# Optimization experiments

Hardware: AMD Instinct MI355X
Metric: run time of the kernel (lower is better)

The kernel has to match this reference:

```python
import jax, jax.numpy as jnp
import numpy as np

DEPTH = 2
TWO_PI = 6.283185307179586


def _apply_ry(state, theta, axis):
    """Apply RY(theta) on qubit at `axis` of state [N,2,2,2,2]. theta: [N] or scalar."""
    half = theta * 0.5
    a0 = jnp.take(state, 0, axis=axis)  # [N,2,2,2]
    a1 = jnp.take(state, 1, axis=axis)
    c = jnp.reshape(jnp.cos(half), (-1,) + (1,) * (a0.ndim - 1))
    s = jnp.reshape(jnp.sin(half), (-1,) + (1,) * (a0.ndim - 1))
    return jnp.stack([c * a0 - s * a1, s * a0 + c * a1], axis=axis)


def _apply_cnot(state, c_axis, t_axis):
    a0 = jnp.take(state, 0, axis=c_axis)  # control=0: unchanged
    a1 = jnp.take(state, 1, axis=c_axis)  # control=1: flip target
    t_ax = t_axis - (1 if t_axis > c_axis else 0)
    a1 = jnp.flip(a1, axis=t_ax)
    return jnp.stack([a0, a1], axis=c_axis)


def _simulate(patches, weights):
    """patches: [N,4] angles. Returns <Z_i> for i=0..3, shape [N,4]. All gates real."""
    N = patches.shape[0]
    state = jnp.zeros((N, 2, 2, 2, 2), dtype=patches.dtype)
    state = state.at[:, 0, 0, 0, 0].set(1.0)
    for w in range(4):  # data encoding
        state = _apply_ry(state, patches[:, w], axis=w + 1)
    for d in range(DEPTH):  # variational layers
        for w in range(4):
            state = _apply_ry(state, weights[d, w], axis=w + 1)
        for c, t in ((0, 1), (1, 2), (2, 3)):
            state = _apply_cnot(state, c + 1, t + 1)
    probs = state * state
    zs = []
    for w in range(4):
        p0 = jnp.take(probs, 0, axis=w + 1).sum(axis=(1, 2, 3))
        p1 = jnp.take(probs, 1, axis=w + 1).sum(axis=(1, 2, 3))
        zs.append(p0 - p1)
    return jnp.stack(zs, axis=-1)  # [N,4]


def setup_inputs() -> dict:
    key = jax.random.key(0)
    k1, k2, k3, k4 = jax.random.split(key, 4)
    B = 8192
    x = jax.random.uniform(k1, (B, 1, 28, 28), dtype=jnp.float32)
    weights = jax.random.uniform(k2, (DEPTH, 4), dtype=jnp.float32) * TWO_PI
    W = jax.random.normal(k3, (10, 4 * 14 * 14), dtype=jnp.float32) * 0.02
    b = jax.random.normal(k4, (10,), dtype=jnp.float32) * 0.02
    return {"x": x, "weights": weights, "W": W, "b": b}


def reference(x, weights, W, b):
    B = x.shape[0]
    # Extract non-overlapping 2x2 patches in row-major (i,j) order;
    # within a patch, order is [(i,j),(i,j+1),(i+1,j),(i+1,j+1)] matching x[:,:,i:i+2,j:j+2].view(B,4)
    p = x.reshape(B, 14, 2, 14, 2).transpose(0, 1, 3, 2, 4).reshape(B, 196, 4)
    feats = _simulate(p.reshape(B * 196, 4), weights).reshape(B, 196 * 4)
    logits = feats @ W.T + b
    return jax.nn.log_softmax(logits, axis=-1)
```

## Files before the change

### kernel.cpp

```cpp
#include <hip/hip_runtime.h>
#include <math.h>

#define INV2PI 0.15915494309189535f

__device__ __forceinline__ float rfl(float v) {
    return __int_as_float(__builtin_amdgcn_readfirstlane(__float_as_int(v)));
}

__global__ __launch_bounds__(256) void quanv_wave_kernel(
    const float* __restrict__ x,
    const float* __restrict__ wts,
    const float* __restrict__ W,
    const float* __restrict__ bias,
    float* __restrict__ out,
    int B)
{
    const int lane = threadIdx.x & 63;
    const int img  = blockIdx.x * 4 + (threadIdx.x >> 6);
    if (img >= B) return;

    float w0r[4], cw1[4], sw1[4];
#pragma unroll
    for (int q = 0; q < 4; ++q) {
        w0r[q] = rfl(wts[q] * INV2PI);
        float r = wts[4 + q] * INV2PI;
        r -= floorf(r);
        cw1[q] = __builtin_amdgcn_cosf(r);
        sw1[q] = __builtin_amdgcn_sinf(r);
    }
    const float cc  = cw1[0]*cw1[1], cs = cw1[0]*sw1[1];
    const float sc  = sw1[0]*cw1[1], ss = sw1[0]*sw1[1];
    const float ccc = cc*cw1[2], ccs = cc*sw1[2], csc = cs*cw1[2], css = cs*sw1[2];
    const float scc = sc*cw1[2], ssc = ss*cw1[2], sss = ss*sw1[2];
    const float K0 = rfl(cw1[0]),       K1 = rfl(-sw1[0]);
    const float K2 = rfl(cc),           K3 = rfl(-cs),          K4 = rfl(ss);
    const float K5 = rfl(ccc),          K6 = rfl(-ccs),         K7 = rfl(css);
    const float K8 = rfl(-scc),         K9 = rfl(-sss);
    const float L1 = rfl(ccc*cw1[3]),   L2 = rfl(-ccc*sw1[3]);
    const float L3 = rfl(ccs*sw1[3]),   L4 = rfl(-csc*cw1[3]);
    const float L5 = rfl(-css*sw1[3]),  L6 = rfl(scc*sw1[3]);
    const float L7 = rfl(ssc*cw1[3]),   L8 = rfl(sss*sw1[3]);

    const float* xim = x + (size_t)img * 784;

    float acc[10];
#pragma unroll
    for (int cl = 0; cl < 10; ++cl) acc[cl] = 0.f;

#pragma unroll
    for (int i = 0; i < 4; ++i) {
        const int p = i * 64 + lane;
        if (p < 196) {
            const int pi = p / 14, pj = p - pi * 14;
            const float* xp = xim + pi * 56 + pj * 2;
            const float2 t0 = *(const float2*)xp;
            const float2 t1 = *(const float2*)(xp + 28);

            float r;
            r = fmaf(t0.x, INV2PI, w0r[0]); r -= floorf(r);
            const float a  = __builtin_amdgcn_sinf(r), A  = __builtin_amdgcn_cosf(r);
            r = fmaf(t0.y, INV2PI, w0r[1]); r -= floorf(r);
            const float b  = __builtin_amdgcn_sinf(r), Bv = __builtin_amdgcn_cosf(r);
            r = fmaf(t1.x, INV2PI, w0r[2]); r -= floorf(r);
            const float c  = __builtin_amdgcn_sinf(r), C  = __builtin_amdgcn_cosf(r);
            r = fmaf(t1.y, INV2PI, w0r[3]); r -= floorf(r);
            const float d  = __builtin_amdgcn_sinf(r), D  = __builtin_amdgcn_cosf(r);

            const float ab=a*b, bc=b*c, ac=a*c, cd=c*d, bd=b*d, ad=a*d;
            const float AC=A*C, Ab=A*b, Bc=Bv*c, BD=Bv*D, cD=c*D, Cd=C*d;

            const float z0 = fmaf(K0, A,  K1*ab);
            const float z1 = fmaf(K2, Bv, fmaf(K3, A*bc, K4*ac));
            const float z2 = fmaf(K5, AC, fmaf(K6, Bv*cd,
                             fmaf(K7, A*bd, fmaf(K8, ab*C, K9*ad))));
            const float z3 = fmaf(L1, BD, fmaf(L2, AC*d, fmaf(L3, Bc,
                             fmaf(L4, Ab*cD, fmaf(L5, Ab, fmaf(L6, ab*Cd,
                             fmaf(L7, ac*D, L8*a)))))));

            const float* wp = W + p * 4;
#pragma unroll
            for (int cl = 0; cl < 10; ++cl) {
                const float4 wv = *(const float4*)(wp + cl * 784);
                acc[cl] = fmaf(z0, wv.x, fmaf(z1, wv.y,
                          fmaf(z2, wv.z, fmaf(z3, wv.w, acc[cl]))));
            }
        }
    }

#pragma unroll
    for (int cl = 0; cl < 10; ++cl) {
        acc[cl] += __shfl_xor(acc[cl], 1, 64);
        acc[cl] += __shfl_xor(acc[cl], 2, 64);
        acc[cl] += __shfl_xor(acc[cl], 4, 64);
        acc[cl] += __shfl_xor(acc[cl], 8, 64);
        acc[cl] += __shfl_xor(acc[cl], 16, 64);
        acc[cl] += __shfl_xor(acc[cl], 32, 64);
        acc[cl] += bias[cl];
    }

    float m = acc[0];
#pragma unroll
    for (int cl = 1; cl < 10; ++cl) m = fmaxf(m, acc[cl]);
    float s = 0.f;
#pragma unroll
    for (int cl = 0; cl < 10; ++cl) s += __expf(acc[cl] - m);
    const float lse = m + __logf(s);

    if (lane == 0) {
        float* op = out + (size_t)img * 10;
        *(float2*)(op + 0) = make_float2(acc[0] - lse, acc[1] - lse);
        *(float2*)(op + 2) = make_float2(acc[2] - lse, acc[3] - lse);
        *(float2*)(op + 4) = make_float2(acc[4] - lse, acc[5] - lse);
        *(float2*)(op + 6) = make_float2(acc[6] - lse, acc[7] - lse);
        *(float2*)(op + 8) = make_float2(acc[8] - lse, acc[9] - lse);
    }
}

extern "C" void kernel_launch(void* const* d_in, const int* in_sizes, int n_in,
                              void* d_out, int out_size, void* d_ws, size_t ws_size,
                              hipStream_t stream) {
    const float* x    = (const float*)d_in[0];
    const float* wts  = (const float*)d_in[1];
    const float* W    = (const float*)d_in[2];
    const float* bias = (const float*)d_in[3];
    float* out        = (float*)d_out;

    const int B = in_sizes[0] / 784;
    const int blocks = (B + 3) / 4;
    quanv_wave_kernel<<<blocks, 256, 0, stream>>>(x, wts, W, bias, out, B);
}
```

Measured before the change: 19.26 us.

## Process four images per wavefront to reuse W loads across images

```diff
diff --git a/kernel.cpp b/kernel.cpp
--- a/kernel.cpp
+++ b/kernel.cpp
@@ -7,7 +7,7 @@
     return __int_as_float(__builtin_amdgcn_readfirstlane(__float_as_int(v)));
 }
 
-__global__ __launch_bounds__(256) void quanv_wave_kernel(
+__global__ __launch_bounds__(256) void quanv_w4_kernel(
     const float* __restrict__ x,
     const float* __restrict__ wts,
     const float* __restrict__ W,
@@ -15,9 +15,9 @@
     float* __restrict__ out,
     int B)
 {
-    const int lane = threadIdx.x & 63;
-    const int img  = blockIdx.x * 4 + (threadIdx.x >> 6);
-    if (img >= B) return;
+    const int lane  = threadIdx.x & 63;
+    const int img0  = (blockIdx.x * 4 + (threadIdx.x >> 6)) * 4;
+    if (img0 >= B) return;
 
     float w0r[4], cw1[4], sw1[4];
 #pragma unroll
@@ -41,78 +41,93 @@
     const float L5 = rfl(-css*sw1[3]),  L6 = rfl(scc*sw1[3]);
     const float L7 = rfl(ssc*cw1[3]),   L8 = rfl(sss*sw1[3]);
 
-    const float* xim = x + (size_t)img * 784;
-
-    float acc[10];
+    float acc[4][10];
 #pragma unroll
-    for (int cl = 0; cl < 10; ++cl) acc[cl] = 0.f;
+    for (int im = 0; im < 4; ++im)
+#pragma unroll
+        for (int cl = 0; cl < 10; ++cl) acc[im][cl] = 0.f;
 
 #pragma unroll
     for (int i = 0; i < 4; ++i) {
         const int p = i * 64 + lane;
         if (p < 196) {
             const int pi = p / 14, pj = p - pi * 14;
-            const float* xp = xim + pi * 56 + pj * 2;
-            const float2 t0 = *(const float2*)xp;
-            const float2 t1 = *(const float2*)(xp + 28);
+            const int xoff = pi * 56 + pj * 2;
 
-            float r;
-            r = fmaf(t0.x, INV2PI, w0r[0]); r -= floorf(r);
-            const float a  = __builtin_amdgcn_sinf(r), A  = __builtin_amdgcn_cosf(r);
-            r = fmaf(t0.y, INV2PI, w0r[1]); r -= floorf(r);
-            const float b  = __builtin_amdgcn_sinf(r), Bv = __builtin_amdgcn_cosf(r);
-            r = fmaf(t1.x, INV2PI, w0r[2]); r -= floorf(r);
-            const float c  = __builtin_amdgcn_sinf(r), C  = __builtin_amdgcn_cosf(r);
-            r = fmaf(t1.y, INV2PI, w0r[3]); r -= floorf(r);
-            const float d  = __builtin_amdgcn_sinf(r), D  = __builtin_amdgcn_cosf(r);
+            float4 wv[10];
+#pragma unroll
+            for (int cl = 0; cl < 10; ++cl)
+                wv[cl] = *(const float4*)(W + cl * 784 + p * 4);
 
-            const float ab=a*b, bc=b*c, ac=a*c, cd=c*d, bd=b*d, ad=a*d;
-            const float AC=A*C, Ab=A*b, Bc=Bv*c, BD=Bv*D, cD=c*D, Cd=C*d;
+#pragma unroll
+            for (int im = 0; im < 4; ++im) {
+                if (img0 + im < B) {
+                    const float* xp = x + (size_t)(img0 + im) * 784 + xoff;
+                    const float2 t0 = *(const float2*)xp;
+                    const float2 t1 = *(const float2*)(xp + 28);
 
-            const float z0 = fmaf(K0, A,  K1*ab);
-            const float z1 = fmaf(K2, Bv, fmaf(K3, A*bc, K4*ac));
-            const float z2 = fmaf(K5, AC, fmaf(K6, Bv*cd,
-                             fmaf(K7, A*bd, fmaf(K8, ab*C, K9*ad))));
-            const float z3 = fmaf(L1, BD, fmaf(L2, AC*d, fmaf(L3, Bc,
-                             fmaf(L4, Ab*cD, fmaf(L5, Ab, fmaf(L6, ab*Cd,
-                             fmaf(L7, ac*D, L8*a)))))));
+                    float r;
+                    r = fmaf(t0.x, INV2PI, w0r[0]); r -= floorf(r);
+                    const float a  = __builtin_amdgcn_sinf(r), A  = __builtin_amdgcn_cosf(r);
+                    r = fmaf(t0.y, INV2PI, w0r[1]); r -= floorf(r);
+                    const float b  = __builtin_amdgcn_sinf(r), Bv = __builtin_amdgcn_cosf(r);
+                    r = fmaf(t1.x, INV2PI, w0r[2]); r -= floorf(r);
+                    const float c  = __builtin_amdgcn_sinf(r), C  = __builtin_amdgcn_cosf(r);
+                    r = fmaf(t1.y, INV2PI, w0r[3]); r -= floorf(r);
+                    const float d  = __builtin_amdgcn_sinf(r), D  = __builtin_amdgcn_cosf(r);
 
-            const float* wp = W + p * 4;
+                    const float ab=a*b, bc=b*c, ac=a*c, cd=c*d, bd=b*d, ad=a*d;
+                    const float AC=A*C, Ab=A*b, Bc=Bv*c, BD=Bv*D, cD=c*D, Cd=C*d;
+
+                    const float z0 = fmaf(K0, A,  K1*ab);
+                    const float z1 = fmaf(K2, Bv, fmaf(K3, A*bc, K4*ac));
+                    const float z2 = fmaf(K5, AC, fmaf(K6, Bv*cd,
+                                     fmaf(K7, A*bd, fmaf(K8, ab*C, K9*ad))));
+                    const float z3 = fmaf(L1, BD, fmaf(L2, AC*d, fmaf(L3, Bc,
+                                     fmaf(L4, Ab*cD, fmaf(L5, Ab, fmaf(L6, ab*Cd,
+                                     fmaf(L7, ac*D, L8*a)))))));
+
 #pragma unroll
-            for (int cl = 0; cl < 10; ++cl) {
-                const float4 wv = *(const float4*)(wp + cl * 784);
-                acc[cl] = fmaf(z0, wv.x, fmaf(z1, wv.y,
-                          fmaf(z2, wv.z, fmaf(z3, wv.w, acc[cl]))));
+                    for (int cl = 0; cl < 10; ++cl)
+                        acc[im][cl] = fmaf(z0, wv[cl].x, fmaf(z1, wv[cl].y,
+                                      fmaf(z2, wv[cl].z, fmaf(z3, wv[cl].w, acc[im][cl]))));
+                }
             }
         }
     }
 
 #pragma unroll
-    for (int cl = 0; cl < 10; ++cl) {
-        acc[cl] += __shfl_xor(acc[cl], 1, 64);
-        acc[cl] += __shfl_xor(acc[cl], 2, 64);
-        acc[cl] += __shfl_xor(acc[cl], 4, 64);
-        acc[cl] += __shfl_xor(acc[cl], 8, 64);
-        acc[cl] += __shfl_xor(acc[cl], 16, 64);
-        acc[cl] += __shfl_xor(acc[cl], 32, 64);
-        acc[cl] += bias[cl];
-    }
+    for (int im = 0; im < 4; ++im) {
+        if (img0 + im < B) {
+            float lg[10];
+#pragma unroll
+            for (int cl = 0; cl < 10; ++cl) {
+                float v = acc[im][cl];
+                v += __shfl_xor(v, 1, 64);
+                v += __shfl_xor(v, 2, 64);
+                v += __shfl_xor(v, 4, 64);
+                v += __shfl_xor(v, 8, 64);
+                v += __shfl_xor(v, 16, 64);
+                v += __shfl_xor(v, 32, 64);
+                lg[cl] = v + bias[cl];
+            }
+            float m = lg[0];
+#pragma unroll
+            for (int cl = 1; cl < 10; ++cl) m = fmaxf(m, lg[cl]);
+            float s = 0.f;
+#pragma unroll
+            for (int cl = 0; cl < 10; ++cl) s += __expf(lg[cl] - m);
+            const float lse = m + __logf(s);
 
-    float m = acc[0];
-#pragma unroll
-    for (int cl = 1; cl < 10; ++cl) m = fmaxf(m, acc[cl]);
-    float s = 0.f;
-#pragma unroll
-    for (int cl = 0; cl < 10; ++cl) s += __expf(acc[cl] - m);
-    const float lse = m + __logf(s);
-
-    if (lane == 0) {
-        float* op = out + (size_t)img * 10;
-        *(float2*)(op + 0) = make_float2(acc[0] - lse, acc[1] - lse);
-        *(float2*)(op + 2) = make_float2(acc[2] - lse, acc[3] - lse);
-        *(float2*)(op + 4) = make_float2(acc[4] - lse, acc[5] - lse);
-        *(float2*)(op + 6) = make_float2(acc[6] - lse, acc[7] - lse);
-        *(float2*)(op + 8) = make_float2(acc[8] - lse, acc[9] - lse);
+            if (lane == 0) {
+                float* op = out + (size_t)(img0 + im) * 10;
+                *(float2*)(op + 0) = make_float2(lg[0] - lse, lg[1] - lse);
+                *(float2*)(op + 2) = make_float2(lg[2] - lse, lg[3] - lse);
+                *(float2*)(op + 4) = make_float2(lg[4] - lse, lg[5] - lse);
+                *(float2*)(op + 6) = make_float2(lg[6] - lse, lg[7] - lse);
+                *(float2*)(op + 8) = make_float2(lg[8] - lse, lg[9] - lse);
+            }
+        }
     }
 }
 
@@ -126,6 +141,6 @@
     float* out        = (float*)d_out;
 
     const int B = in_sizes[0] / 784;
-    const int blocks = (B + 3) / 4;
-    quanv_wave_kernel<<<blocks, 256, 0, stream>>>(x, wts, W, bias, out, B);
+    const int blocks = (B + 15) / 16;
+    quanv_w4_kernel<<<blocks, 256, 0, stream>>>(x, wts, W, bias, out, B);
 }
```

Result: slower. 20.29 us (+5.4%).

## Remap work so each lane handles a patch pair across four images

Applied to the files above, without the earlier changes.

```diff
diff --git a/kernel.cpp b/kernel.cpp
--- a/kernel.cpp
+++ b/kernel.cpp
@@ -7,7 +7,7 @@
     return __int_as_float(__builtin_amdgcn_readfirstlane(__float_as_int(v)));
 }
 
-__global__ __launch_bounds__(256) void quanv_wave_kernel(
+__global__ __launch_bounds__(448) void quanv_pair_kernel(
     const float* __restrict__ x,
     const float* __restrict__ wts,
     const float* __restrict__ W,
@@ -15,9 +15,26 @@
     float* __restrict__ out,
     int B)
 {
-    const int lane = threadIdx.x & 63;
-    const int img  = blockIdx.x * 4 + (threadIdx.x >> 6);
-    if (img >= B) return;
+    __shared__ float part[7][4][10];
+    __shared__ float logits[4][10];
+
+    const int tid   = threadIdx.x;
+    const int wave  = tid >> 6, lane = tid & 63;
+    const int im_l  = lane & 3;
+    const int pslot = lane >> 2;
+    const int im_g  = blockIdx.x * 4 + im_l;
+    const bool act  = (pslot < 14) && (im_g < B);
+
+    const int pair = wave * 14 + pslot;
+    const int pi   = pair / 7;
+    const int pj   = pair - pi * 7;
+
+    float4 xt = make_float4(0.f, 0.f, 0.f, 0.f), xb = xt;
+    if (act) {
+        const float* xp = x + (size_t)im_g * 784 + pi * 56 + pj * 4;
+        xt = *(const float4*)xp;
+        xb = *(const float4*)(xp + 28);
+    }
 
     float w0r[4], cw1[4], sw1[4];
 #pragma unroll
@@ -41,78 +58,86 @@
     const float L5 = rfl(-css*sw1[3]),  L6 = rfl(scc*sw1[3]);
     const float L7 = rfl(ssc*cw1[3]),   L8 = rfl(sss*sw1[3]);
 
-    const float* xim = x + (size_t)img * 784;
+    float z[2][4];
+#pragma unroll
+    for (int h = 0; h < 2; ++h) {
+        const float t0 = h ? xt.z : xt.x;
+        const float t1 = h ? xt.w : xt.y;
+        const float t2 = h ? xb.z : xb.x;
+        const float t3 = h ? xb.w : xb.y;
+
+        float r;
+        r = fmaf(t0, INV2PI, w0r[0]); r -= floorf(r);
+        const float a  = __builtin_amdgcn_sinf(r), A  = __builtin_amdgcn_cosf(r);
+        r = fmaf(t1, INV2PI, w0r[1]); r -= floorf(r);
+        const float b  = __builtin_amdgcn_sinf(r), Bv = __builtin_amdgcn_cosf(r);
+        r = fmaf(t2, INV2PI, w0r[2]); r -= floorf(r);
+        const float c  = __builtin_amdgcn_sinf(r), C  = __builtin_amdgcn_cosf(r);
+        r = fmaf(t3, INV2PI, w0r[3]); r -= floorf(r);
+        const float d  = __builtin_amdgcn_sinf(r), D  = __builtin_amdgcn_cosf(r);
+
+        const float ab=a*b, bc=b*c, ac=a*c, cd=c*d, bd=b*d, ad=a*d;
+        const float AC=A*C, Ab=A*b, Bc=Bv*c, BD=Bv*D, cD=c*D, Cd=C*d;
+
+        z[h][0] = fmaf(K0, A,  K1*ab);
+        z[h][1] = fmaf(K2, Bv, fmaf(K3, A*bc, K4*ac));
+        z[h][2] = fmaf(K5, AC, fmaf(K6, Bv*cd,
+                  fmaf(K7, A*bd, fmaf(K8, ab*C, K9*ad))));
+        z[h][3] = fmaf(L1, BD, fmaf(L2, AC*d, fmaf(L3, Bc,
+                  fmaf(L4, Ab*cD, fmaf(L5, Ab, fmaf(L6, ab*Cd,
+                  fmaf(L7, ac*D, L8*a)))))));
+    }
 
     float acc[10];
 #pragma unroll
     for (int cl = 0; cl < 10; ++cl) acc[cl] = 0.f;
 
+    if (act) {
+        const int kL = pi * 56 + pj * 8;
 #pragma unroll
-    for (int i = 0; i < 4; ++i) {
-        const int p = i * 64 + lane;
-        if (p < 196) {
-            const int pi = p / 14, pj = p - pi * 14;
-            const float* xp = xim + pi * 56 + pj * 2;
-            const float2 t0 = *(const float2*)xp;
-            const float2 t1 = *(const float2*)(xp + 28);
-
-            float r;
-            r = fmaf(t0.x, INV2PI, w0r[0]); r -= floorf(r);
-            const float a  = __builtin_amdgcn_sinf(r), A  = __builtin_amdgcn_cosf(r);
-            r = fmaf(t0.y, INV2PI, w0r[1]); r -= floorf(r);
-            const float b  = __builtin_amdgcn_sinf(r), Bv = __builtin_amdgcn_cosf(r);
-            r = fmaf(t1.x, INV2PI, w0r[2]); r -= floorf(r);
-            const float c  = __builtin_amdgcn_sinf(r), C  = __builtin_amdgcn_cosf(r);
-            r = fmaf(t1.y, INV2PI, w0r[3]); r -= floorf(r);
-            const float d  = __builtin_amdgcn_sinf(r), D  = __builtin_amdgcn_cosf(r);
-
-            const float ab=a*b, bc=b*c, ac=a*c, cd=c*d, bd=b*d, ad=a*d;
-            const float AC=A*C, Ab=A*b, Bc=Bv*c, BD=Bv*D, cD=c*D, Cd=C*d;
-
-            const float z0 = fmaf(K0, A,  K1*ab);
-            const float z1 = fmaf(K2, Bv, fmaf(K3, A*bc, K4*ac));
-            const float z2 = fmaf(K5, AC, fmaf(K6, Bv*cd,
-                             fmaf(K7, A*bd, fmaf(K8, ab*C, K9*ad))));
-            const float z3 = fmaf(L1, BD, fmaf(L2, AC*d, fmaf(L3, Bc,
-                             fmaf(L4, Ab*cD, fmaf(L5, Ab, fmaf(L6, ab*Cd,
-                             fmaf(L7, ac*D, L8*a)))))));
-
-            const float* wp = W + p * 4;
-#pragma unroll
-            for (int cl = 0; cl < 10; ++cl) {
-                const float4 wv = *(const float4*)(wp + cl * 784);
-                acc[cl] = fmaf(z0, wv.x, fmaf(z1, wv.y,
-                          fmaf(z2, wv.z, fmaf(z3, wv.w, acc[cl]))));
-            }
+        for (int cl = 0; cl < 10; ++cl) {
+            const float* wp = W + cl * 784 + kL;
+            const float4 wvL = *(const float4*)wp;
+            const float4 wvR = *(const float4*)(wp + 4);
+            acc[cl] = fmaf(z[0][0], wvL.x, fmaf(z[0][1], wvL.y,
+                      fmaf(z[0][2], wvL.z, fmaf(z[0][3], wvL.w,
+                      fmaf(z[1][0], wvR.x, fmaf(z[1][1], wvR.y,
+                      fmaf(z[1][2], wvR.z, fmaf(z[1][3], wvR.w, acc[cl]))))))));
         }
     }
 
 #pragma unroll
     for (int cl = 0; cl < 10; ++cl) {
-        acc[cl] += __shfl_xor(acc[cl], 1, 64);
-        acc[cl] += __shfl_xor(acc[cl], 2, 64);
-        acc[cl] += __shfl_xor(acc[cl], 4, 64);
-        acc[cl] += __shfl_xor(acc[cl], 8, 64);
-        acc[cl] += __shfl_xor(acc[cl], 16, 64);
-        acc[cl] += __shfl_xor(acc[cl], 32, 64);
-        acc[cl] += bias[cl];
+        float v = acc[cl];
+        v += __shfl_xor(v, 4, 64);
+        v += __shfl_xor(v, 8, 64);
+        v += __shfl_xor(v, 16, 64);
+        v += __shfl_xor(v, 32, 64);
+        if (lane < 4) part[wave][lane][cl] = v;
     }
+    __syncthreads();
 
-    float m = acc[0];
+    if (tid < 40) {
+        const int im = tid / 10, cl = tid - (tid / 10) * 10;
+        float s = bias[cl];
 #pragma unroll
-    for (int cl = 1; cl < 10; ++cl) m = fmaxf(m, acc[cl]);
-    float s = 0.f;
+        for (int w = 0; w < 7; ++w) s += part[w][im][cl];
+        logits[im][cl] = s;
+    }
+    __syncthreads();
+
+    if (tid < 40) {
+        const int im = tid / 10, cl = tid - (tid / 10) * 10;
+        const int img = blockIdx.x * 4 + im;
+        if (img < B) {
+            float m = logits[im][0];
 #pragma unroll
-    for (int cl = 0; cl < 10; ++cl) s += __expf(acc[cl] - m);
-    const float lse = m + __logf(s);
-
-    if (lane == 0) {
-        float* op = out + (size_t)img * 10;
-        *(float2*)(op + 0) = make_float2(acc[0] - lse, acc[1] - lse);
-        *(float2*)(op + 2) = make_float2(acc[2] - lse, acc[3] - lse);
-        *(float2*)(op + 4) = make_float2(acc[4] - lse, acc[5] - lse);
-        *(float2*)(op + 6) = make_float2(acc[6] - lse, acc[7] - lse);
-        *(float2*)(op + 8) = make_float2(acc[8] - lse, acc[9] - lse);
+            for (int j = 1; j < 10; ++j) m = fmaxf(m, logits[im][j]);
+            float s = 0.f;
+#pragma unroll
+            for (int j = 0; j < 10; ++j) s += __expf(logits[im][j] - m);
+            out[(size_t)img * 10 + cl] = logits[im][cl] - m - __logf(s);
+        }
     }
 }
 
@@ -127,5 +152,5 @@
 
     const int B = in_sizes[0] / 784;
     const int blocks = (B + 3) / 4;
-    quanv_wave_kernel<<<blocks, 256, 0, stream>>>(x, wts, W, bias, out, B);
+    quanv_pair_kernel<<<blocks, 448, 0, stream>>>(x, wts, W, bias, out, B);
 }
```

Measured after the change: 19.88 us. 3.2% more time.
